# Kernel optimization log

Measured on AMD Instinct MI355X. Metric: run time of the kernel, lower is better.

Reference implementation:

```python
import jax, jax.numpy as jnp
import numpy as np

NEG_SLOPE = 0.2
EPS = 1e-10

B, N, F_IN = 2, 20000, 128
H, D = 4, 32
E = 640000


def setup_inputs() -> dict:
    key = jax.random.key(0)
    k1, k2, k3, k4, k5 = jax.random.split(key, 5)
    x = jax.random.normal(k1, (B, N, F_IN), dtype=jnp.float32)
    edge_index = jax.random.randint(k2, (2, E), 0, N, dtype=jnp.int64)
    W = jax.random.normal(k3, (H * D, F_IN), dtype=jnp.float32) * (1.0 / np.sqrt(F_IN))
    a_src = jax.random.normal(k4, (H, D), dtype=jnp.float32) * (1.0 / np.sqrt(D))
    a_dst = jax.random.normal(k5, (H, D), dtype=jnp.float32) * (1.0 / np.sqrt(D))
    return {"x": x, "edge_index": edge_index, "W": W, "a_src": a_src, "a_dst": a_dst}


def reference(x, edge_index, W, a_src, a_dst):
    # x: (B, N, F_IN); edge_index: (2, E); W: (H*D, F_IN)
    Bs, Ns, _ = x.shape
    h = (x @ W.T).reshape(Bs, Ns, H, D)          # (B, N, H, D)
    src = edge_index[0]
    dst = edge_index[1]

    h_src = h[:, src]                            # (B, E, H, D) gather
    e_src = jnp.einsum('behd,hd->beh', h_src, a_src)
    e_dst = jnp.einsum('behd,hd->beh', h[:, dst], a_dst)
    e = jax.nn.leaky_relu(e_src + e_dst, NEG_SLOPE)  # (B, E, H)

    # segment softmax over destination nodes (segments on leading axis)
    e_t = jnp.moveaxis(e, 1, 0)                  # (E, B, H)
    max_n = jax.ops.segment_max(e_t, dst, num_segments=Ns)   # (N, B, H)
    exp_e = jnp.exp(e_t - max_n[dst])            # (E, B, H)
    sum_n = jax.ops.segment_sum(exp_e, dst, num_segments=Ns)  # (N, B, H)
    alpha = exp_e / (sum_n[dst] + EPS)           # (E, B, H)

    messages = alpha[..., None] * jnp.moveaxis(h_src, 1, 0)  # (E, B, H, D)
    out = jax.ops.segment_sum(messages, dst, num_segments=Ns)  # (N, B, H, D)
    out = jnp.moveaxis(out, 0, 1).reshape(Bs, Ns, H * D)       # concat heads
    return out
```

## Files before the change

kernel.cpp:

```cpp
#include <hip/hip_runtime.h>
#include <math.h>

#define N_NODES 20000
#define N_B 2
#define N_H 4
#define N_D 32
#define N_F 128
#define N_E 640000
#define BNH (N_B * N_NODES * N_H)

#define GEMM_BLOCKS 625
#define P1_BLOCKS 250
#define EPB 2560
#define NBINS 157
#define BINCAP 4608
#define NODE_CAP 96
#define TRS 136
#define LOG2E 1.44269504088896f

typedef __attribute__((ext_vector_type(8))) short short8v;
typedef __attribute__((ext_vector_type(4))) float floatx4;

__device__ __forceinline__ unsigned short f2bf(float f) {
  unsigned u = __float_as_uint(f);
  return (unsigned short)((u + 0x7FFFu + ((u >> 16) & 1u)) >> 16);
}

__global__ __launch_bounds__(256) void fused_gemm_p1(
    const float* __restrict__ X, const float* __restrict__ W,
    const int* __restrict__ EI, const float* __restrict__ a_src,
    const float* __restrict__ a_dst, unsigned short* __restrict__ HbI,
    float* __restrict__ sI, float* __restrict__ sdI, int* __restrict__ gbin,
    unsigned* __restrict__ coarse) {
  __shared__ unsigned short WbS[128 * 128];
  __shared__ unsigned short Tr[4][16 * TRS];
  __shared__ int hist[NBINS], base[NBINS], hist2[NBINS];
  const int tid = threadIdx.x;

  if (blockIdx.x >= GEMM_BLOCKS) {
    const int e0 = (blockIdx.x - GEMM_BLOCKS) * EPB;
    if (tid < NBINS) { hist[tid] = 0; hist2[tid] = 0; }
    __syncthreads();
    for (int k = 0; k < EPB; k += 256) {
      const int dst = EI[N_E + e0 + k + tid];
      atomicAdd(&hist[dst >> 7], 1);
    }
    __syncthreads();
    if (tid < NBINS) base[tid] = hist[tid] ? atomicAdd(&gbin[tid], hist[tid]) : 0;
    __syncthreads();
    for (int k = 0; k < EPB; k += 256) {
      const int i = e0 + k + tid;
      const int dst = EI[N_E + i];
      const int src = EI[i];
      const int bin = dst >> 7;
      const int pos = base[bin] + atomicAdd(&hist2[bin], 1);
      if (pos < BINCAP)
        coarse[bin * BINCAP + pos] = (unsigned)(((dst & 127) << 16) | src);
    }
    return;
  }

  {
    const int o = tid >> 1;
    const int khalf = (tid & 1) * 64;
#pragma unroll
    for (int c = 0; c < 8; ++c) {
      const int k0 = khalf + c * 8;
      const float4 w0 = *(const float4*)&W[(size_t)o * 128 + k0];
      const float4 w1 = *(const float4*)&W[(size_t)o * 128 + k0 + 4];
      union { unsigned short us[8]; uint4 v; } pk;
      pk.us[0] = f2bf(w0.x); pk.us[1] = f2bf(w0.y);
      pk.us[2] = f2bf(w0.z); pk.us[3] = f2bf(w0.w);
      pk.us[4] = f2bf(w1.x); pk.us[5] = f2bf(w1.y);
      pk.us[6] = f2bf(w1.z); pk.us[7] = f2bf(w1.w);
      const int chunk = (k0 >> 3) ^ (o & 15);
      *(uint4*)&WbS[o * 128 + chunk * 8] = pk.v;
    }
  }
  __syncthreads();

  const int wv = tid >> 6, lane = tid & 63;
  const int l15 = lane & 15;
  const int row0 = blockIdx.x * 64 + wv * 16;
  const int arow = row0 + l15;
  const int kg = lane >> 4;

  float as[8], ad[8];
#pragma unroll
  for (int cf = 0; cf < 8; ++cf) {
    as[cf] = a_src[cf * 16 + l15];
    ad[cf] = a_dst[cf * 16 + l15];
  }

  short8v afr[4];
#pragma unroll
  for (int kc = 0; kc < 4; ++kc) {
    const size_t xb = (size_t)arow * 128 + kc * 32 + kg * 8;
    const float4 x0 = *(const float4*)&X[xb];
    const float4 x1 = *(const float4*)&X[xb + 4];
    afr[kc][0] = (short)f2bf(x0.x); afr[kc][1] = (short)f2bf(x0.y);
    afr[kc][2] = (short)f2bf(x0.z); afr[kc][3] = (short)f2bf(x0.w);
    afr[kc][4] = (short)f2bf(x1.x); afr[kc][5] = (short)f2bf(x1.y);
    afr[kc][6] = (short)f2bf(x1.z); afr[kc][7] = (short)f2bf(x1.w);
  }

  floatx4 acc[8];
#pragma unroll
  for (int cf = 0; cf < 8; ++cf) acc[cf] = (floatx4){0.f, 0.f, 0.f, 0.f};

#pragma unroll
  for (int kc = 0; kc < 4; ++kc) {
#pragma unroll
    for (int cf = 0; cf < 8; ++cf) {
      const int o = cf * 16 + l15;
      const int chunk = (kc * 4 + kg) ^ l15;
      const short8v bfr = *(const short8v*)&WbS[o * 128 + chunk * 8];
      acc[cf] = __builtin_amdgcn_mfma_f32_16x16x32_bf16(afr[kc], bfr, acc[cf], 0, 0, 0);
    }
  }

  {
    float ps[4][4], pd[4][4];
#pragma unroll
    for (int j = 0; j < 4; ++j)
#pragma unroll
      for (int h = 0; h < 4; ++h) {
        float vs = acc[2 * h][j] * as[2 * h] + acc[2 * h + 1][j] * as[2 * h + 1];
        float vd = acc[2 * h][j] * ad[2 * h] + acc[2 * h + 1][j] * ad[2 * h + 1];
#pragma unroll
        for (int m = 1; m <= 8; m <<= 1) {
          vs += __shfl_xor(vs, m);
          vd += __shfl_xor(vd, m);
        }
        ps[j][h] = vs * LOG2E; pd[j][h] = vd * LOG2E;
      }
    if (l15 == 0) {
#pragma unroll
      for (int j = 0; j < 4; ++j) {
        const int m = row0 + kg * 4 + j;
        const int node = (m < N_NODES) ? m : m - N_NODES;
        const int boff = (m < N_NODES) ? 0 : 4;
#pragma unroll
        for (int h = 0; h < 4; ++h) {
          sI[node * 8 + boff + h] = ps[j][h];
          sdI[node * 8 + boff + h] = pd[j][h];
        }
      }
    }
  }

#pragma unroll
  for (int cf = 0; cf < 8; ++cf)
#pragma unroll
    for (int j = 0; j < 4; ++j)
      Tr[wv][((kg << 2) + j) * TRS + cf * 16 + l15] = f2bf(acc[cf][j]);
#pragma unroll
  for (int it = 0; it < 4; ++it) {
    const int r = it * 4 + kg;
    const int m = row0 + r;
    const size_t base2 =
        (m < N_NODES) ? (size_t)m * 256 : (size_t)(m - N_NODES) * 256 + 128;
    const uint4 v = *(const uint4*)&Tr[wv][r * TRS + l15 * 8];
    *(uint4*)&HbI[base2 + l15 * 8] = v;
  }
}

__global__ __launch_bounds__(256) void bin_kernel(
    const unsigned* __restrict__ coarse, const int* __restrict__ gbin,
    unsigned short* __restrict__ bucket, int* __restrict__ count) {
  __shared__ unsigned short list[128][NODE_CAP];
  __shared__ int cnt[128];
  const int bin = blockIdx.x;
  const int tid = threadIdx.x;
  if (tid < 128) cnt[tid] = 0;
  __syncthreads();
  const int n = min(gbin[bin], BINCAP);
  for (int k = tid; k < n; k += 256) {
    const unsigned p = coarse[bin * BINCAP + k];
    const int dl = (int)(p >> 16);
    const int r = atomicAdd(&cnt[dl], 1);
    if (r < NODE_CAP) list[dl][r] = (unsigned short)(p & 0xFFFFu);
  }
  __syncthreads();
  const int dl = tid >> 1, half = tid & 1;
  const int node = bin * 128 + dl;
  if (node < N_NODES) {
    const int c = min(cnt[dl], NODE_CAP);
    if (half == 0) count[node] = c;
#pragma unroll
    for (int q = 0; q < 6; ++q) {
      const int off = (half * 6 + q) * 8;
      if (off < c)
        *(uint4*)&bucket[(size_t)node * NODE_CAP + off] =
            *(const uint4*)&list[dl][off];
    }
  }
}

__global__ __launch_bounds__(256) void agg_kernel(
    const unsigned short* __restrict__ HbI, const float* __restrict__ sI,
    const float* __restrict__ sdI, const int* __restrict__ count,
    const unsigned short* __restrict__ bucket, float* __restrict__ out) {
  const int node = blockIdx.x * 4 + (threadIdx.x >> 6);
  const int lane = threadIdx.x & 63;
  const int j = (lane >> 3) & 7;

  const uint2* __restrict__ Hu2 = (const uint2*)HbI;
  const int cnt = count[node];
  const float sd = sdI[node * 8 + j];
  const int bbase = node * NODE_CAP;

  float den = 0.f, a0 = 0.f, a1 = 0.f, a2 = 0.f, a3 = 0.f;

#define COMP(h_, f_)                                                \
  {                                                                 \
    float lg = (f_) + sd;                                           \
    lg = fmaxf(lg, 0.2f * lg);                                      \
    const float p = exp2f(lg);                                      \
    den += p;                                                       \
    a0 = fmaf(p, __uint_as_float((h_).x << 16), a0);                \
    a1 = fmaf(p, __uint_as_float((h_).x & 0xFFFF0000u), a1);        \
    a2 = fmaf(p, __uint_as_float((h_).y << 16), a2);                \
    a3 = fmaf(p, __uint_as_float((h_).y & 0xFFFF0000u), a3);        \
  }

  for (int cb = 0; cb < cnt; cb += 64) {
    const int c = min(cnt - cb, 64);
    const int vE = (lane < c) ? (int)bucket[bbase + cb + lane] : 0;
    int e = 0;
    for (; e + 4 <= c; e += 4) {
      const int sA = __shfl(vE, e), sB = __shfl(vE, e + 1);
      const int sC = __shfl(vE, e + 2), sD = __shfl(vE, e + 3);
      const uint2 hA = Hu2[(size_t)sA * 64 + lane];
      const uint2 hB = Hu2[(size_t)sB * 64 + lane];
      const uint2 hC = Hu2[(size_t)sC * 64 + lane];
      const uint2 hD = Hu2[(size_t)sD * 64 + lane];
      const float fA = sI[sA * 8 + j], fB = sI[sB * 8 + j];
      const float fC = sI[sC * 8 + j], fD = sI[sD * 8 + j];
      COMP(hA, fA) COMP(hB, fB) COMP(hC, fC) COMP(hD, fD)
    }
    for (; e < c; ++e) {
      const int sA = __shfl(vE, e);
      const uint2 hA = Hu2[(size_t)sA * 64 + lane];
      const float fA = sI[sA * 8 + j];
      COMP(hA, fA)
    }
  }
#undef COMP

  const float inv = 1.f / (den + 1e-10f);
  float4 o;
  o.x = a0 * inv; o.y = a1 * inv; o.z = a2 * inv; o.w = a3 * inv;
  *(float4*)&out[(size_t)(lane >> 5) * (N_NODES * 128) + (size_t)node * 128 +
                 (lane & 31) * 4] = o;
}

extern "C" void kernel_launch(void* const* d_in, const int* in_sizes, int n_in,
                              void* d_out, int out_size, void* d_ws, size_t ws_size,
                              hipStream_t stream) {
  const float* X = (const float*)d_in[0];
  const int* EI = (const int*)d_in[1];
  const float* W = (const float*)d_in[2];
  const float* a_src = (const float*)d_in[3];
  const float* a_dst = (const float*)d_in[4];
  float* out = (float*)d_out;

  unsigned short* hbI = (unsigned short*)d_ws;
  float* sI = (float*)(hbI + (size_t)N_B * N_NODES * N_F);
  float* sdI = sI + BNH;
  int* gbin = (int*)(sdI + BNH);
  unsigned* coarse = (unsigned*)(gbin + 160);
  int* count = (int*)(coarse + (size_t)NBINS * BINCAP);
  unsigned short* bucket = (unsigned short*)(count + N_NODES);

  hipMemsetAsync(gbin, 0, NBINS * sizeof(int), stream);
  fused_gemm_p1<<<GEMM_BLOCKS + P1_BLOCKS, 256, 0, stream>>>(
      X, W, EI, a_src, a_dst, hbI, sI, sdI, gbin, coarse);
  bin_kernel<<<NBINS, 256, 0, stream>>>(coarse, gbin, bucket, count);
  agg_kernel<<<N_NODES / 4, 256, 0, stream>>>(hbI, sI, sdI, count, bucket, out);
}
```

Measured before the change: 82.10 us.

## Replace global bin atomics with per-block sorted edge lists; split aggregation per batch-head

The edge-binning pass now counting-sorts each block's edges by destination bin in shared memory and writes per-block counts, prefixes and sorted edges, so no global atomics or memset are needed. The bin kernel then has each thread walk one source block's segment for its bin. The aggregation kernel is split into 8 times more blocks, one per (batch, head) slice, with four edges processed in parallel per wave and a cross-lane reduction at the end. This adds parallelism and removes the bin capacity limit, but the bin kernel's serial per-thread walk over at most 250 segments may be unbalanced, and the redundant bucket and index reads across 8 slices add traffic.

```diff
diff --git a/kernel.cpp b/kernel.cpp
--- a/kernel.cpp
+++ b/kernel.cpp
@@ -13,7 +13,6 @@
 #define P1_BLOCKS 250
 #define EPB 2560
 #define NBINS 157
-#define BINCAP 4608
 #define NODE_CAP 96
 #define TRS 136
 #define LOG2E 1.44269504088896f
@@ -30,33 +29,71 @@
     const float* __restrict__ X, const float* __restrict__ W,
     const int* __restrict__ EI, const float* __restrict__ a_src,
     const float* __restrict__ a_dst, unsigned short* __restrict__ HbI,
-    float* __restrict__ sI, float* __restrict__ sdI, int* __restrict__ gbin,
-    unsigned* __restrict__ coarse) {
-  __shared__ unsigned short WbS[128 * 128];
-  __shared__ unsigned short Tr[4][16 * TRS];
-  __shared__ int hist[NBINS], base[NBINS], hist2[NBINS];
+    float* __restrict__ sI, float* __restrict__ sdI,
+    int* __restrict__ cntB, int* __restrict__ prefB,
+    unsigned* __restrict__ blockEdges) {
+  __shared__ union {
+    struct {
+      unsigned short WbS[128 * 128];
+      unsigned short Tr[4][16 * TRS];
+    } g;
+    struct {
+      int hist[NBINS];
+      int pref[NBINS];
+      int wsum[4];
+      unsigned buf[EPB];
+    } p;
+  } sm;
   const int tid = threadIdx.x;
 
   if (blockIdx.x >= GEMM_BLOCKS) {
-    const int e0 = (blockIdx.x - GEMM_BLOCKS) * EPB;
-    if (tid < NBINS) { hist[tid] = 0; hist2[tid] = 0; }
+    const int pb = blockIdx.x - GEMM_BLOCKS;
+    const int e0 = pb * EPB;
+    for (int t = tid; t < NBINS; t += 256) sm.p.hist[t] = 0;
     __syncthreads();
     for (int k = 0; k < EPB; k += 256) {
-      const int dst = EI[N_E + e0 + k + tid];
-      atomicAdd(&hist[dst >> 7], 1);
+      const int d = EI[N_E + e0 + k + tid];
+      atomicAdd(&sm.p.hist[d >> 7], 1);
     }
     __syncthreads();
-    if (tid < NBINS) base[tid] = hist[tid] ? atomicAdd(&gbin[tid], hist[tid]) : 0;
+    {
+      const int w = tid >> 6, lane = tid & 63;
+      int v = 0, incl = 0;
+      if (tid < NBINS) v = sm.p.hist[tid];
+      if (w < 3) {
+        incl = v;
+#pragma unroll
+        for (int off = 1; off < 64; off <<= 1) {
+          int t2 = __shfl_up(incl, off);
+          if (lane >= off) incl += t2;
+        }
+        if (lane == 63) sm.p.wsum[w] = incl;
+      }
+      __syncthreads();
+      if (tid < NBINS) {
+        int add = 0;
+        if (w >= 1) add += sm.p.wsum[0];
+        if (w >= 2) add += sm.p.wsum[1];
+        sm.p.pref[tid] = incl - v + add;
+      }
+      __syncthreads();
+    }
+    for (int t = tid; t < NBINS; t += 256) {
+      cntB[pb * NBINS + t] = sm.p.hist[t];
+      prefB[pb * NBINS + t] = sm.p.pref[t];
+      sm.p.hist[t] = sm.p.pref[t];
+    }
     __syncthreads();
     for (int k = 0; k < EPB; k += 256) {
       const int i = e0 + k + tid;
-      const int dst = EI[N_E + i];
-      const int src = EI[i];
-      const int bin = dst >> 7;
-      const int pos = base[bin] + atomicAdd(&hist2[bin], 1);
-      if (pos < BINCAP)
-        coarse[bin * BINCAP + pos] = (unsigned)(((dst & 127) << 16) | src);
-    }
+      const int d = EI[N_E + i];
+      const int s = EI[i];
+      const int pos = atomicAdd(&sm.p.hist[d >> 7], 1);
+      sm.p.buf[pos] = (unsigned)(((d & 127) << 16) | s);
+    }
+    __syncthreads();
+    for (int k = tid; k < EPB; k += 256)
+      blockEdges[(size_t)pb * EPB + k] = sm.p.buf[k];
     return;
   }
 
@@ -74,7 +111,7 @@
       pk.us[4] = f2bf(w1.x); pk.us[5] = f2bf(w1.y);
       pk.us[6] = f2bf(w1.z); pk.us[7] = f2bf(w1.w);
       const int chunk = (k0 >> 3) ^ (o & 15);
-      *(uint4*)&WbS[o * 128 + chunk * 8] = pk.v;
+      *(uint4*)&sm.g.WbS[o * 128 + chunk * 8] = pk.v;
     }
   }
   __syncthreads();
@@ -114,7 +151,7 @@
     for (int cf = 0; cf < 8; ++cf) {
       const int o = cf * 16 + l15;
       const int chunk = (kc * 4 + kg) ^ l15;
-      const short8v bfr = *(const short8v*)&WbS[o * 128 + chunk * 8];
+      const short8v bfr = *(const short8v*)&sm.g.WbS[o * 128 + chunk * 8];
       acc[cf] = __builtin_amdgcn_mfma_f32_16x16x32_bf16(afr[kc], bfr, acc[cf], 0, 0, 0);
     }
   }
@@ -153,33 +190,38 @@
   for (int cf = 0; cf < 8; ++cf)
 #pragma unroll
     for (int j = 0; j < 4; ++j)
-      Tr[wv][((kg << 2) + j) * TRS + cf * 16 + l15] = f2bf(acc[cf][j]);
+      sm.g.Tr[wv][((kg << 2) + j) * TRS + cf * 16 + l15] = f2bf(acc[cf][j]);
 #pragma unroll
   for (int it = 0; it < 4; ++it) {
     const int r = it * 4 + kg;
     const int m = row0 + r;
     const size_t base2 =
         (m < N_NODES) ? (size_t)m * 256 : (size_t)(m - N_NODES) * 256 + 128;
-    const uint4 v = *(const uint4*)&Tr[wv][r * TRS + l15 * 8];
+    const uint4 v = *(const uint4*)&sm.g.Tr[wv][r * TRS + l15 * 8];
     *(uint4*)&HbI[base2 + l15 * 8] = v;
   }
 }
 
 __global__ __launch_bounds__(256) void bin_kernel(
-    const unsigned* __restrict__ coarse, const int* __restrict__ gbin,
-    unsigned short* __restrict__ bucket, int* __restrict__ count) {
+    const unsigned* __restrict__ blockEdges, const int* __restrict__ cntB,
+    const int* __restrict__ prefB, unsigned short* __restrict__ bucket,
+    int* __restrict__ count) {
   __shared__ unsigned short list[128][NODE_CAP];
   __shared__ int cnt[128];
   const int bin = blockIdx.x;
   const int tid = threadIdx.x;
   if (tid < 128) cnt[tid] = 0;
   __syncthreads();
-  const int n = min(gbin[bin], BINCAP);
-  for (int k = tid; k < n; k += 256) {
-    const unsigned p = coarse[bin * BINCAP + k];
-    const int dl = (int)(p >> 16);
-    const int r = atomicAdd(&cnt[dl], 1);
-    if (r < NODE_CAP) list[dl][r] = (unsigned short)(p & 0xFFFFu);
+  for (int b = tid; b < P1_BLOCKS; b += 256) {
+    const int c = cntB[b * NBINS + bin];
+    const int p0 = prefB[b * NBINS + bin];
+    const size_t base = (size_t)b * EPB + p0;
+    for (int q = 0; q < c; ++q) {
+      const unsigned u = blockEdges[base + q];
+      const int dl = (int)(u >> 16);
+      const int r = atomicAdd(&cnt[dl], 1);
+      if (r < NODE_CAP) list[dl][r] = (unsigned short)(u & 0xFFFFu);
+    }
   }
   __syncthreads();
   const int dl = tid >> 1, half = tid & 1;
@@ -198,61 +240,49 @@
 }
 
 __global__ __launch_bounds__(256) void agg_kernel(
-    const unsigned short* __restrict__ HbI, const float* __restrict__ sI,
+    const unsigned* __restrict__ Hu, const float* __restrict__ sI,
     const float* __restrict__ sdI, const int* __restrict__ count,
     const unsigned short* __restrict__ bucket, float* __restrict__ out) {
-  const int node = blockIdx.x * 4 + (threadIdx.x >> 6);
+  const int s = blockIdx.x & 7;
+  const int node = (blockIdx.x >> 3) * 4 + (threadIdx.x >> 6);
   const int lane = threadIdx.x & 63;
-  const int j = (lane >> 3) & 7;
-
-  const uint2* __restrict__ Hu2 = (const uint2*)HbI;
+  const int l15 = lane & 15;
+  const int eg = lane >> 4;
+
   const int cnt = count[node];
-  const float sd = sdI[node * 8 + j];
+  const float sd = sdI[node * 8 + s];
   const int bbase = node * NODE_CAP;
-
-  float den = 0.f, a0 = 0.f, a1 = 0.f, a2 = 0.f, a3 = 0.f;
-
-#define COMP(h_, f_)                                                \
-  {                                                                 \
-    float lg = (f_) + sd;                                           \
-    lg = fmaxf(lg, 0.2f * lg);                                      \
-    const float p = exp2f(lg);                                      \
-    den += p;                                                       \
-    a0 = fmaf(p, __uint_as_float((h_).x << 16), a0);                \
-    a1 = fmaf(p, __uint_as_float((h_).x & 0xFFFF0000u), a1);        \
-    a2 = fmaf(p, __uint_as_float((h_).y << 16), a2);                \
-    a3 = fmaf(p, __uint_as_float((h_).y & 0xFFFF0000u), a3);        \
-  }
+  const int hoff = s * 16 + l15;
+
+  float den = 0.f, a0 = 0.f, a1 = 0.f;
 
   for (int cb = 0; cb < cnt; cb += 64) {
     const int c = min(cnt - cb, 64);
     const int vE = (lane < c) ? (int)bucket[bbase + cb + lane] : 0;
-    int e = 0;
-    for (; e + 4 <= c; e += 4) {
-      const int sA = __shfl(vE, e), sB = __shfl(vE, e + 1);
-      const int sC = __shfl(vE, e + 2), sD = __shfl(vE, e + 3);
-      const uint2 hA = Hu2[(size_t)sA * 64 + lane];
-      const uint2 hB = Hu2[(size_t)sB * 64 + lane];
-      const uint2 hC = Hu2[(size_t)sC * 64 + lane];
-      const uint2 hD = Hu2[(size_t)sD * 64 + lane];
-      const float fA = sI[sA * 8 + j], fB = sI[sB * 8 + j];
-      const float fC = sI[sC * 8 + j], fD = sI[sD * 8 + j];
-      COMP(hA, fA) COMP(hB, fB) COMP(hC, fC) COMP(hD, fD)
-    }
-    for (; e < c; ++e) {
-      const int sA = __shfl(vE, e);
-      const uint2 hA = Hu2[(size_t)sA * 64 + lane];
-      const float fA = sI[sA * 8 + j];
-      COMP(hA, fA)
-    }
-  }
-#undef COMP
-
-  const float inv = 1.f / (den + 1e-10f);
-  float4 o;
-  o.x = a0 * inv; o.y = a1 * inv; o.z = a2 * inv; o.w = a3 * inv;
-  *(float4*)&out[(size_t)(lane >> 5) * (N_NODES * 128) + (size_t)node * 128 +
-                 (lane & 31) * 4] = o;
+#pragma unroll 2
+    for (int e = 0; e < c; e += 4) {
+      const int eo = e + eg;
+      const int src = __shfl(vE, eo);
+      float lg = sI[src * 8 + s] + sd;
+      lg = fmaxf(lg, 0.2f * lg);
+      const float p = (eo < c) ? exp2f(lg) : 0.f;
+      const unsigned h = Hu[(size_t)src * 128 + hoff];
+      den += p;
+      a0 = fmaf(p, __uint_as_float(h << 16), a0);
+      a1 = fmaf(p, __uint_as_float(h & 0xFFFF0000u), a1);
+    }
+  }
+
+  a0 += __shfl_xor(a0, 16); a0 += __shfl_xor(a0, 32);
+  a1 += __shfl_xor(a1, 16); a1 += __shfl_xor(a1, 32);
+  den += __shfl_xor(den, 16); den += __shfl_xor(den, 32);
+
+  if (lane < 16) {
+    const float inv = 1.f / (den + 1e-10f);
+    const int b = s >> 2, h = s & 3;
+    *(float2*)&out[(size_t)b * (N_NODES * 128) + (size_t)node * 128 + h * 32 +
+                   l15 * 2] = make_float2(a0 * inv, a1 * inv);
+  }
 }
 
 extern "C" void kernel_launch(void* const* d_in, const int* in_sizes, int n_in,
@@ -268,14 +298,15 @@
   unsigned short* hbI = (unsigned short*)d_ws;
   float* sI = (float*)(hbI + (size_t)N_B * N_NODES * N_F);
   float* sdI = sI + BNH;
-  int* gbin = (int*)(sdI + BNH);
-  unsigned* coarse = (unsigned*)(gbin + 160);
-  int* count = (int*)(coarse + (size_t)NBINS * BINCAP);
+  int* cntB = (int*)(sdI + BNH);
+  int* prefB = cntB + P1_BLOCKS * NBINS;
+  unsigned* blockEdges = (unsigned*)(prefB + P1_BLOCKS * NBINS);
+  int* count = (int*)(blockEdges + (size_t)N_E);
   unsigned short* bucket = (unsigned short*)(count + N_NODES);
 
-  hipMemsetAsync(gbin, 0, NBINS * sizeof(int), stream);
   fused_gemm_p1<<<GEMM_BLOCKS + P1_BLOCKS, 256, 0, stream>>>(
-      X, W, EI, a_src, a_dst, hbI, sI, sdI, gbin, coarse);
-  bin_kernel<<<NBINS, 256, 0, stream>>>(coarse, gbin, bucket, count);
-  agg_kernel<<<N_NODES / 4, 256, 0, stream>>>(hbI, sI, sdI, count, bucket, out);
-}
+      X, W, EI, a_src, a_dst, hbI, sI, sdI, cntB, prefB, blockEdges);
+  bin_kernel<<<NBINS, 256, 0, stream>>>(blockEdges, cntB, prefB, bucket, count);
+  agg_kernel<<<(N_NODES / 4) * 8, 256, 0, stream>>>(
+      (const unsigned*)hbI, sI, sdI, count, bucket, out);
+}
```

Result: slower. 124.1 us (+51.2%).
